# Kernel optimization log

Measured on AMD Instinct MI355X. Metric: run time of the kernel, lower is better.

Reference implementation:

```python
import jax, jax.numpy as jnp
import numpy as np

INPUT_DIM = 4
HIDDEN_DIM = 256
T_OBS, T_UNOBS, BATCH = 64, 32, 4096


def setup_inputs() -> dict:
    key = jax.random.key(0)
    ks = jax.random.split(key, 16)
    H, D = HIDDEN_DIM, INPUT_DIM
    s = lambda k, shape, fan: jax.random.normal(k, shape, jnp.float32) * (1.0 / np.sqrt(fan))
    return {
        "x_obs": jax.random.normal(ks[0], (T_OBS, BATCH, D), jnp.float32),
        "t_obs": jnp.cumsum(jax.random.uniform(ks[1], (T_OBS, BATCH, 1), jnp.float32), axis=0),
        "t_unobs": jax.random.uniform(ks[2], (T_UNOBS, BATCH, 1), jnp.float32),
        # stem MLP (n_layers=2): Linear(D+1 -> H), LeakyReLU, Linear(H -> H)
        "stem_w1": s(ks[3], (H, D + 1), D + 1),
        "stem_b1": jnp.zeros((H,), jnp.float32),
        "stem_w2": s(ks[4], (H, H), H),
        "stem_b2": jnp.zeros((H,), jnp.float32),
        # single-layer GRU, PyTorch gate order (r, z, n)
        "gru_wi": s(ks[5], (3 * H, H), H),
        "gru_wh": s(ks[6], (3 * H, H), H),
        "gru_bi": jnp.zeros((3 * H,), jnp.float32),
        "gru_bh": jnp.zeros((3 * H,), jnp.float32),
        # head MLP (n_layers=1): Linear(H -> D)
        "head_w": s(ks[7], (D, H), H),
        "head_b": jnp.zeros((D,), jnp.float32),
    }


def _gru_cell(x, h, wi, wh, bi, bh):
    # x, h: [B, H].  PyTorch GRU: r,z gates sigmoid; n gate tanh with r gating hidden path.
    gx = x @ wi.T + bi
    gh = h @ wh.T + bh
    rx, zx, nx = jnp.split(gx, 3, axis=-1)
    rh, zh, nh = jnp.split(gh, 3, axis=-1)
    r = jax.nn.sigmoid(rx + rh)
    u = jax.nn.sigmoid(zx + zh)
    n = jnp.tanh(nx + r * nh)
    return (1.0 - u) * n + u * h


def reference(x_obs, t_obs, t_unobs, stem_w1, stem_b1, stem_w2, stem_b2,
              gru_wi, gru_wh, gru_bi, gru_bh, head_w, head_b):
    unobs_len = t_unobs.shape[0]
    batch, hidden = x_obs.shape[1], gru_wh.shape[1]

    # preprocess: first difference of time (0 at step 0), concat, stem MLP
    t_diff = jnp.concatenate([jnp.zeros_like(t_obs[:1]), t_obs[1:] - t_obs[:-1]], axis=0)
    xt = jnp.concatenate([x_obs, t_diff], axis=-1)             # [T_obs, B, D+1]
    xt = jax.nn.leaky_relu(xt @ stem_w1.T + stem_b1)
    xt = xt @ stem_w2.T + stem_b2                              # [T_obs, B, H]

    cell = lambda x, h: _gru_cell(x, jax.lax.stop_gradient(h), gru_wi, gru_wh, gru_bi, gru_bh)

    h0 = jnp.zeros((batch, hidden), x_obs.dtype)

    def obs_step(h, x_t):
        h_new = cell(x_t, h)
        return h_new, None

    h, _ = jax.lax.scan(obs_step, h0, xt)
    z_last = h                                                  # output of 1-layer GRU == hidden

    def ar_step(carry, _):
        z, h = carry
        h_new = cell(z, h)
        return (h_new, h_new), h_new

    (_, _), zs_rest = jax.lax.scan(ar_step, (z_last, h), None, length=unobs_len - 1)
    zs = jnp.concatenate([z_last[None], zs_rest], axis=0)       # [T_unobs, B, H]

    x_hats = zs @ head_w.T + head_b                             # [T_unobs, B, D]
    return x_hats, zs
```

## Files before the change

### kernel.cpp

```cpp
#include <hip/hip_runtime.h>
#include <cstdint>
#include <cstddef>

#define T_OBS_C 64
#define T_UNOBS_C 32
#define BATCH_C 4096
#define HID_C 256

typedef short v8s __attribute__((ext_vector_type(8)));
typedef float v4f __attribute__((ext_vector_type(4)));
typedef unsigned short u16x8 __attribute__((ext_vector_type(8)));

__device__ __forceinline__ float bf2f(unsigned short u) {
  union { unsigned int i; float f; } v; v.i = ((unsigned int)u) << 16; return v.f;
}
__device__ __forceinline__ unsigned short f2bf(float f) {
  union { float f; unsigned int i; } v; v.f = f;
  unsigned int r = (v.i + 0x7FFFu + ((v.i >> 16) & 1u)) >> 16;
  return (unsigned short)r;
}

__global__ void prep_kernel(const float* __restrict__ wi,
                            const float* __restrict__ w2,
                            const float* __restrict__ b2,
                            const float* __restrict__ bi,
                            unsigned short* __restrict__ wi_hi,
                            unsigned short* __restrict__ wi_lo,
                            const float* __restrict__ wh,
                            unsigned short* __restrict__ wh_hi,
                            unsigned short* __restrict__ wh_lo,
                            unsigned short* __restrict__ wc_hi,
                            unsigned short* __restrict__ wc_lo,
                            float* __restrict__ bc_obs) {
  const int n = blockIdx.x;
  const int k = threadIdx.x;
  const int idx = n * 256 + k;

  float wv = wi[idx];
  unsigned short h1 = f2bf(wv);
  wi_hi[idx] = h1; wi_lo[idx] = f2bf(wv - bf2f(h1));

  float hv = wh[idx];
  unsigned short h2 = f2bf(hv);
  wh_hi[idx] = h2; wh_lo[idx] = f2bf(hv - bf2f(h2));

  float acc = 0.f;
  for (int j = 0; j < 256; ++j)
    acc += wi[n * 256 + j] * w2[j * 256 + k];
  unsigned short h3 = f2bf(acc);
  wc_hi[idx] = h3; wc_lo[idx] = f2bf(acc - bf2f(h3));

  if (k == 0) {
    float b = 0.f;
    for (int j = 0; j < 256; ++j) b += wi[n * 256 + j] * b2[j];
    bc_obs[n] = b + bi[n];
  }
}

__global__ __launch_bounds__(512, 2)
void rnn_xcd(const float* __restrict__ x_obs,
             const float* __restrict__ t_obs,
             const float* __restrict__ w1,
             const float* __restrict__ b1,
             const unsigned short* __restrict__ wc_hi, const unsigned short* __restrict__ wc_lo,
             const unsigned short* __restrict__ wi_hi, const unsigned short* __restrict__ wi_lo,
             const unsigned short* __restrict__ wh_hi, const unsigned short* __restrict__ wh_lo,
             const float* __restrict__ bc_obs,
             const float* __restrict__ bi,
             const float* __restrict__ bh,
             const float* __restrict__ head_w,
             const float* __restrict__ head_b,
             unsigned short* h_hi0, unsigned short* h_lo0,
             unsigned short* h_hi1, unsigned short* h_lo1,
             unsigned short* st_hi0, unsigned short* st_lo0,
             unsigned short* st_hi1, unsigned short* st_lo1,
             unsigned int* cnt,
             float* out_x,
             float* out_z) {
  __shared__ unsigned short wlds[73728];

  const int tid = threadIdx.x;
  const int bid = blockIdx.x;
  const int jj  = bid & 15;
  const int cg  = bid >> 4;
  const int rg  = ((jj & 7) << 1) | (jj >> 3);
  const int m0  = rg << 8;
  const int c0  = cg << 4;

  {
    const unsigned short* srcs[6] = {wc_hi, wc_lo, wi_hi, wi_lo, wh_hi, wh_lo};
    for (int id = tid; id < 9216; id += 512) {
      const int sub = id >> 9;
      const int mat = sub / 6;
      const int g   = (sub >> 1) % 3;
      const int hl  = sub & 1;
      const int within = id & 511;
      const int row = within >> 5;
      const int c16 = within & 31;
      const unsigned short* s = srcs[mat * 2 + hl] +
          (((size_t)(g * 256 + c0 + row)) << 8) + (c16 << 3);
      u16x8 v = *(const u16x8*)s;
      *(u16x8*)(wlds + (sub << 12) + (row << 8) + ((c16 ^ row) << 3)) = v;
    }
  }

  const int wave = tid >> 6;
  const int lane = tid & 63;
  const int quad = lane >> 4;
  const int l16  = lane & 15;
  const int jc   = c0 + l16;

  float xb_o[3], xb_a[3], hb_[3], hwv[4];
  #pragma unroll
  for (int g = 0; g < 3; ++g) {
    xb_o[g] = bc_obs[g * 256 + jc];
    xb_a[g] = bi[g * 256 + jc];
    hb_[g]  = bh[g * 256 + jc];
  }
  #pragma unroll
  for (int d = 0; d < 4; ++d) hwv[d] = head_w[d * 256 + jc];

  const size_t rowA0 = (size_t)(m0 + (wave * 2 + 0) * 16 + l16) << 8;
  const size_t rowA1 = (size_t)(m0 + (wave * 2 + 1) * 16 + l16) << 8;

  auto stem_slice = [&](int tt, unsigned short* dh, unsigned short* dl) {
    const int row  = tid >> 1;
    const int half = tid & 1;
    const size_t grow = (size_t)(m0 + row);
    const size_t xo = (size_t)tt * BATCH_C + grow;
    const float4 xv = *(const float4*)(x_obs + xo * 4);
    float td = 0.f;
    if (tt > 0) td = t_obs[xo] - t_obs[xo - BATCH_C];
    const int j0 = c0 + half * 8;
    u16x8 hi8, lo8;
    #pragma unroll
    for (int j = 0; j < 8; ++j) {
      const int jg = j0 + j;
      const float* wr = w1 + jg * 5;
      float pre = xv.x * wr[0] + xv.y * wr[1] + xv.z * wr[2] +
                  xv.w * wr[3] + td * wr[4] + b1[jg];
      float a = (pre > 0.f) ? pre : 0.01f * pre;
      unsigned short h = f2bf(a);
      hi8[j] = h; lo8[j] = f2bf(a - bf2f(h));
    }
    *(u16x8*)(dh + (grow << 8) + j0) = hi8;
    *(u16x8*)(dl + (grow << 8) + j0) = lo8;
  };

  auto rgbar = [&](unsigned int epoch) {
    __syncthreads();
    if (tid == 0) {
      unsigned int* c = cnt + (rg << 6);
      __hip_atomic_fetch_add(c, 1u, __ATOMIC_RELEASE, __HIP_MEMORY_SCOPE_AGENT);
      const unsigned int tgt = epoch << 4;
      while (__hip_atomic_load(c, __ATOMIC_ACQUIRE, __HIP_MEMORY_SCOPE_AGENT) < tgt)
        __builtin_amdgcn_s_sleep(2);
    }
    __syncthreads();
  };

  stem_slice(0, st_hi0, st_lo0);
  rgbar(1);

  unsigned int epoch = 2;
  #pragma unroll 1
  for (int step = 0; step < T_OBS_C + T_UNOBS_C - 1; ++step) {
    const bool obs = (step < T_OBS_C);
    const unsigned short* hih = (step & 1) ? h_hi1 : h_hi0;
    const unsigned short* hil = (step & 1) ? h_lo1 : h_lo0;
    unsigned short* hoh = (step & 1) ? h_hi0 : h_hi1;
    unsigned short* hol = (step & 1) ? h_lo0 : h_lo1;
    const unsigned short* sxh = obs ? ((step & 1) ? st_hi1 : st_hi0) : hih;
    const unsigned short* sxl = obs ? ((step & 1) ? st_lo1 : st_lo0) : hil;
    const int matx = obs ? 0 : 1;
    const int zi = (step == T_OBS_C - 1) ? 0
                   : (step >= T_OBS_C ? step - (T_OBS_C - 1) : -1);

    v4f aX[2][3], aH[2][3];
    #pragma unroll
    for (int mt = 0; mt < 2; ++mt)
      #pragma unroll
      for (int g = 0; g < 3; ++g) {
        aX[mt][g] = (v4f){0.f, 0.f, 0.f, 0.f};
        aH[mt][g] = (v4f){0.f, 0.f, 0.f, 0.f};
      }

    #pragma unroll
    for (int kc = 0; kc < 8; ++kc) {
      const size_t ko = (size_t)(kc * 32 + quad * 8);
      v8s ax0h = *(const v8s*)(sxh + rowA0 + ko);
      v8s ax0l = *(const v8s*)(sxl + rowA0 + ko);
      v8s ax1h = *(const v8s*)(sxh + rowA1 + ko);
      v8s ax1l = *(const v8s*)(sxl + rowA1 + ko);
      v8s ah0h, ah0l, ah1h, ah1l;
      if (obs) {
        ah0h = *(const v8s*)(hih + rowA0 + ko);
        ah0l = *(const v8s*)(hil + rowA0 + ko);
        ah1h = *(const v8s*)(hih + rowA1 + ko);
        ah1l = *(const v8s*)(hil + rowA1 + ko);
      } else {
        ah0h = ax0h; ah0l = ax0l; ah1h = ax1h; ah1l = ax1l;
      }
      const int lrow = (l16 << 8) + ((((kc * 4 + quad) ^ l16)) << 3);
      #pragma unroll
      for (int g = 0; g < 3; ++g) {
        const v8s bxh = *(const v8s*)(wlds + (((matx * 3 + g) * 2 + 0) << 12) + lrow);
        const v8s bxl = *(const v8s*)(wlds + (((matx * 3 + g) * 2 + 1) << 12) + lrow);
        const v8s bhh = *(const v8s*)(wlds + (((6 + g) * 2 + 0) << 12) + lrow);
        const v8s bhl = *(const v8s*)(wlds + (((6 + g) * 2 + 1) << 12) + lrow);
        aX[0][g] = __builtin_amdgcn_mfma_f32_16x16x32_bf16(ax0h, bxh, aX[0][g], 0, 0, 0);
        aX[0][g] = __builtin_amdgcn_mfma_f32_16x16x32_bf16(ax0l, bxh, aX[0][g], 0, 0, 0);
        aX[0][g] = __builtin_amdgcn_mfma_f32_16x16x32_bf16(ax0h, bxl, aX[0][g], 0, 0, 0);
        aX[1][g] = __builtin_amdgcn_mfma_f32_16x16x32_bf16(ax1h, bxh, aX[1][g], 0, 0, 0);
        aX[1][g] = __builtin_amdgcn_mfma_f32_16x16x32_bf16(ax1l, bxh, aX[1][g], 0, 0, 0);
        aX[1][g] = __builtin_amdgcn_mfma_f32_16x16x32_bf16(ax1h, bxl, aX[1][g], 0, 0, 0);
        aH[0][g] = __builtin_amdgcn_mfma_f32_16x16x32_bf16(ah0h, bhh, aH[0][g], 0, 0, 0);
        aH[0][g] = __builtin_amdgcn_mfma_f32_16x16x32_bf16(ah0l, bhh, aH[0][g], 0, 0, 0);
        aH[0][g] = __builtin_amdgcn_mfma_f32_16x16x32_bf16(ah0h, bhl, aH[0][g], 0, 0, 0);
        aH[1][g] = __builtin_amdgcn_mfma_f32_16x16x32_bf16(ah1h, bhh, aH[1][g], 0, 0, 0);
        aH[1][g] = __builtin_amdgcn_mfma_f32_16x16x32_bf16(ah1l, bhh, aH[1][g], 0, 0, 0);
        aH[1][g] = __builtin_amdgcn_mfma_f32_16x16x32_bf16(ah1h, bhl, aH[1][g], 0, 0, 0);
      }
    }

    #pragma unroll
    for (int mt = 0; mt < 2; ++mt) {
      #pragma unroll
      for (int r = 0; r < 4; ++r) {
        const int grow = m0 + (wave * 2 + mt) * 16 + quad * 4 + r;
        const size_t hoff = ((size_t)grow << 8) + jc;
        const float xbr = obs ? xb_o[0] : xb_a[0];
        const float xbz = obs ? xb_o[1] : xb_a[1];
        const float xbn = obs ? xb_o[2] : xb_a[2];
        float gr = aX[mt][0][r] + xbr + aH[mt][0][r] + hb_[0];
        float gz = aX[mt][1][r] + xbz + aH[mt][1][r] + hb_[1];
        float nx = aX[mt][2][r] + xbn;
        float nh = aH[mt][2][r] + hb_[2];
        float rr = 1.f / (1.f + expf(-gr));
        float uu = 1.f / (1.f + expf(-gz));
        float nn = tanhf(nx + rr * nh);
        float hold = bf2f(hih[hoff]) + bf2f(hil[hoff]);
        float hnew = (1.f - uu) * nn + uu * hold;
        unsigned short hi = f2bf(hnew);
        hoh[hoff] = hi;
        hol[hoff] = f2bf(hnew - bf2f(hi));
        if (zi >= 0) {
          out_z[((size_t)zi << 20) + hoff] = hnew;
          #pragma unroll
          for (int d = 0; d < 4; ++d) {
            float pd = hnew * hwv[d];
            pd += __shfl_xor(pd, 1);
            pd += __shfl_xor(pd, 2);
            pd += __shfl_xor(pd, 4);
            pd += __shfl_xor(pd, 8);
            if (l16 == 0) {
              if (cg == 0) pd += head_b[d];
              atomicAdd(out_x + ((((size_t)zi << 12) + grow) << 2) + d, pd);
            }
          }
        }
      }
    }

    if (obs && step + 1 < T_OBS_C)
      stem_slice(step + 1, ((step + 1) & 1) ? st_hi1 : st_hi0,
                           ((step + 1) & 1) ? st_lo1 : st_lo0);

    if (step < T_OBS_C + T_UNOBS_C - 2) rgbar(epoch++);
  }
}

extern "C" void kernel_launch(void* const* d_in, const int* in_sizes, int n_in,
                              void* d_out, int out_size, void* d_ws, size_t ws_size,
                              hipStream_t stream) {
  const float* x_obs = (const float*)d_in[0];
  const float* t_obs = (const float*)d_in[1];
  const float* w1 = (const float*)d_in[3];
  const float* b1 = (const float*)d_in[4];
  const float* w2 = (const float*)d_in[5];
  const float* b2 = (const float*)d_in[6];
  const float* wi = (const float*)d_in[7];
  const float* wh = (const float*)d_in[8];
  const float* bi = (const float*)d_in[9];
  const float* bh = (const float*)d_in[10];
  const float* hw = (const float*)d_in[11];
  const float* hb = (const float*)d_in[12];

  float* out_x = (float*)d_out;
  float* out_z = out_x + (size_t)T_UNOBS_C * BATCH_C * 4;

  unsigned short* p = (unsigned short*)d_ws;
  unsigned short* wi_hi = p; p += 768 * 256;
  unsigned short* wi_lo = p; p += 768 * 256;
  unsigned short* wh_hi = p; p += 768 * 256;
  unsigned short* wh_lo = p; p += 768 * 256;
  unsigned short* wc_hi = p; p += 768 * 256;
  unsigned short* wc_lo = p; p += 768 * 256;
  unsigned short* h_hi0 = p; p += (size_t)1 << 20;
  unsigned short* h_lo0 = p; p += (size_t)1 << 20;
  unsigned short* h_hi1 = p; p += (size_t)1 << 20;
  unsigned short* h_lo1 = p; p += (size_t)1 << 20;
  unsigned short* st_hi0 = p; p += (size_t)1 << 20;
  unsigned short* st_lo0 = p; p += (size_t)1 << 20;
  unsigned short* st_hi1 = p; p += (size_t)1 << 20;
  unsigned short* st_lo1 = p; p += (size_t)1 << 20;
  float* bc_obs = (float*)p; p += 768 * 2;
  unsigned int* cnt = (unsigned int*)p;

  hipMemsetAsync(h_hi0, 0, (size_t)4 << 20, stream);
  hipMemsetAsync(cnt, 0, 16 * 64 * sizeof(unsigned int), stream);
  hipMemsetAsync(out_x, 0, (size_t)T_UNOBS_C * BATCH_C * 4 * sizeof(float), stream);

  prep_kernel<<<768, 256, 0, stream>>>(wi, w2, b2, bi,
                                       wi_hi, wi_lo, wh, wh_hi, wh_lo,
                                       wc_hi, wc_lo, bc_obs);

  void* args[] = {
    (void*)&x_obs, (void*)&t_obs, (void*)&w1, (void*)&b1,
    (void*)&wc_hi, (void*)&wc_lo, (void*)&wi_hi, (void*)&wi_lo,
    (void*)&wh_hi, (void*)&wh_lo,
    (void*)&bc_obs, (void*)&bi, (void*)&bh, (void*)&hw, (void*)&hb,
    (void*)&h_hi0, (void*)&h_lo0, (void*)&h_hi1, (void*)&h_lo1,
    (void*)&st_hi0, (void*)&st_lo0, (void*)&st_hi1, (void*)&st_lo1,
    (void*)&cnt, (void*)&out_x, (void*)&out_z
  };
  hipLaunchCooperativeKernel(reinterpret_cast<void*>(rnn_xcd),
                             dim3(256), dim3(512), args, 0, stream);
}
```

Before: 3.288 ms.

## Compute stem activations in registers and precompute next-step input projection off critical path

Each wave now computes the stem LeakyReLU activations for its own rows directly in registers, using w1 and b1 copied into shared memory, instead of writing bf16 hi/lo stem slices to global buffers and reading them back. The input-path MFMA accumulation for step t+1 is run after step t's gate update and before the grid barrier, so each observed step only does the hidden-path matmul after the barrier. This removes the global round trip for the stem buffers and shortens the post-barrier critical path. In exchange each wave recomputes the stem for its K slice, and holding the extra aXp accumulators raises register pressure.

```diff
diff --git a/kernel.cpp b/kernel.cpp
--- a/kernel.cpp
+++ b/kernel.cpp
@@ -58,7 +58,7 @@
 }
 
 __global__ __launch_bounds__(512, 2)
-void rnn_xcd(const float* __restrict__ x_obs,
+void rnn_ws2(const float* __restrict__ x_obs,
              const float* __restrict__ t_obs,
              const float* __restrict__ w1,
              const float* __restrict__ b1,
@@ -72,12 +72,12 @@
              const float* __restrict__ head_b,
              unsigned short* h_hi0, unsigned short* h_lo0,
              unsigned short* h_hi1, unsigned short* h_lo1,
-             unsigned short* st_hi0, unsigned short* st_lo0,
-             unsigned short* st_hi1, unsigned short* st_lo1,
              unsigned int* cnt,
              float* out_x,
              float* out_z) {
   __shared__ unsigned short wlds[73728];
+  __shared__ float w1t[1280];
+  __shared__ float b1s[256];
 
   const int tid = threadIdx.x;
   const int bid = blockIdx.x;
@@ -102,6 +102,11 @@
       u16x8 v = *(const u16x8*)s;
       *(u16x8*)(wlds + (sub << 12) + (row << 8) + ((c16 ^ row) << 3)) = v;
     }
+    for (int i = tid; i < 1280; i += 512) {
+      const int k = i / 5, j = i - k * 5;
+      w1t[j * 256 + k] = w1[i];
+    }
+    if (tid < 256) b1s[tid] = b1[tid];
   }
 
   const int wave = tid >> 6;
@@ -120,32 +125,10 @@
   #pragma unroll
   for (int d = 0; d < 4; ++d) hwv[d] = head_w[d * 256 + jc];
 
-  const size_t rowA0 = (size_t)(m0 + (wave * 2 + 0) * 16 + l16) << 8;
-  const size_t rowA1 = (size_t)(m0 + (wave * 2 + 1) * 16 + l16) << 8;
-
-  auto stem_slice = [&](int tt, unsigned short* dh, unsigned short* dl) {
-    const int row  = tid >> 1;
-    const int half = tid & 1;
-    const size_t grow = (size_t)(m0 + row);
-    const size_t xo = (size_t)tt * BATCH_C + grow;
-    const float4 xv = *(const float4*)(x_obs + xo * 4);
-    float td = 0.f;
-    if (tt > 0) td = t_obs[xo] - t_obs[xo - BATCH_C];
-    const int j0 = c0 + half * 8;
-    u16x8 hi8, lo8;
-    #pragma unroll
-    for (int j = 0; j < 8; ++j) {
-      const int jg = j0 + j;
-      const float* wr = w1 + jg * 5;
-      float pre = xv.x * wr[0] + xv.y * wr[1] + xv.z * wr[2] +
-                  xv.w * wr[3] + td * wr[4] + b1[jg];
-      float a = (pre > 0.f) ? pre : 0.01f * pre;
-      unsigned short h = f2bf(a);
-      hi8[j] = h; lo8[j] = f2bf(a - bf2f(h));
-    }
-    *(u16x8*)(dh + (grow << 8) + j0) = hi8;
-    *(u16x8*)(dl + (grow << 8) + j0) = lo8;
-  };
+  const int rowL0 = (wave * 2 + 0) * 16 + l16;
+  const int rowL1 = (wave * 2 + 1) * 16 + l16;
+  const size_t rowA0 = (size_t)(m0 + rowL0) << 8;
+  const size_t rowA1 = (size_t)(m0 + rowL1) << 8;
 
   auto rgbar = [&](unsigned int epoch) {
     __syncthreads();
@@ -159,7 +142,62 @@
     __syncthreads();
   };
 
-  stem_slice(0, st_hi0, st_lo0);
+  __syncthreads();
+
+  float4 xv0, xv1; float td0 = 0.f, td1 = 0.f;
+  auto load_x = [&](int tt) {
+    const size_t xo0 = (size_t)tt * BATCH_C + m0 + rowL0;
+    const size_t xo1 = (size_t)tt * BATCH_C + m0 + rowL1;
+    xv0 = *(const float4*)(x_obs + xo0 * 4);
+    xv1 = *(const float4*)(x_obs + xo1 * 4);
+    if (tt > 0) {
+      td0 = t_obs[xo0] - t_obs[xo0 - BATCH_C];
+      td1 = t_obs[xo1] - t_obs[xo1 - BATCH_C];
+    } else { td0 = 0.f; td1 = 0.f; }
+  };
+
+  v4f aXp[2][3];
+  auto xpath_pre = [&]() {
+    #pragma unroll
+    for (int mt = 0; mt < 2; ++mt)
+      #pragma unroll
+      for (int g = 0; g < 3; ++g)
+        aXp[mt][g] = (v4f){0.f, 0.f, 0.f, 0.f};
+    #pragma unroll
+    for (int kc = 0; kc < 8; ++kc) {
+      v8s s0h, s0l, s1h, s1l;
+      #pragma unroll
+      for (int j = 0; j < 8; ++j) {
+        const int k = kc * 32 + quad * 8 + j;
+        const float wA = w1t[k], wB = w1t[256 + k], wC = w1t[512 + k],
+                    wD = w1t[768 + k], wE = w1t[1024 + k];
+        const float bb = b1s[k];
+        float p0 = xv0.x * wA + xv0.y * wB + xv0.z * wC + xv0.w * wD + td0 * wE + bb;
+        float a0 = (p0 > 0.f) ? p0 : 0.01f * p0;
+        unsigned short h0 = f2bf(a0);
+        s0h[j] = h0; s0l[j] = f2bf(a0 - bf2f(h0));
+        float p1 = xv1.x * wA + xv1.y * wB + xv1.z * wC + xv1.w * wD + td1 * wE + bb;
+        float a1 = (p1 > 0.f) ? p1 : 0.01f * p1;
+        unsigned short h1 = f2bf(a1);
+        s1h[j] = h1; s1l[j] = f2bf(a1 - bf2f(h1));
+      }
+      const int lrow = (l16 << 8) + ((((kc * 4 + quad) ^ l16)) << 3);
+      #pragma unroll
+      for (int g = 0; g < 3; ++g) {
+        const v8s bxh = *(const v8s*)(wlds + ((g * 2 + 0) << 12) + lrow);
+        const v8s bxl = *(const v8s*)(wlds + ((g * 2 + 1) << 12) + lrow);
+        aXp[0][g] = __builtin_amdgcn_mfma_f32_16x16x32_bf16(s0h, bxh, aXp[0][g], 0, 0, 0);
+        aXp[0][g] = __builtin_amdgcn_mfma_f32_16x16x32_bf16(s0l, bxh, aXp[0][g], 0, 0, 0);
+        aXp[0][g] = __builtin_amdgcn_mfma_f32_16x16x32_bf16(s0h, bxl, aXp[0][g], 0, 0, 0);
+        aXp[1][g] = __builtin_amdgcn_mfma_f32_16x16x32_bf16(s1h, bxh, aXp[1][g], 0, 0, 0);
+        aXp[1][g] = __builtin_amdgcn_mfma_f32_16x16x32_bf16(s1l, bxh, aXp[1][g], 0, 0, 0);
+        aXp[1][g] = __builtin_amdgcn_mfma_f32_16x16x32_bf16(s1h, bxl, aXp[1][g], 0, 0, 0);
+      }
+    }
+  };
+
+  load_x(0);
+  xpath_pre();
   rgbar(1);
 
   unsigned int epoch = 2;
@@ -170,9 +208,6 @@
     const unsigned short* hil = (step & 1) ? h_lo1 : h_lo0;
     unsigned short* hoh = (step & 1) ? h_hi0 : h_hi1;
     unsigned short* hol = (step & 1) ? h_lo0 : h_lo1;
-    const unsigned short* sxh = obs ? ((step & 1) ? st_hi1 : st_hi0) : hih;
-    const unsigned short* sxl = obs ? ((step & 1) ? st_lo1 : st_lo0) : hil;
-    const int matx = obs ? 0 : 1;
     const int zi = (step == T_OBS_C - 1) ? 0
                    : (step >= T_OBS_C ? step - (T_OBS_C - 1) : -1);
 
@@ -181,45 +216,62 @@
     for (int mt = 0; mt < 2; ++mt)
       #pragma unroll
       for (int g = 0; g < 3; ++g) {
-        aX[mt][g] = (v4f){0.f, 0.f, 0.f, 0.f};
+        aX[mt][g] = obs ? aXp[mt][g] : (v4f){0.f, 0.f, 0.f, 0.f};
         aH[mt][g] = (v4f){0.f, 0.f, 0.f, 0.f};
       }
 
-    #pragma unroll
-    for (int kc = 0; kc < 8; ++kc) {
-      const size_t ko = (size_t)(kc * 32 + quad * 8);
-      v8s ax0h = *(const v8s*)(sxh + rowA0 + ko);
-      v8s ax0l = *(const v8s*)(sxl + rowA0 + ko);
-      v8s ax1h = *(const v8s*)(sxh + rowA1 + ko);
-      v8s ax1l = *(const v8s*)(sxl + rowA1 + ko);
-      v8s ah0h, ah0l, ah1h, ah1l;
-      if (obs) {
-        ah0h = *(const v8s*)(hih + rowA0 + ko);
-        ah0l = *(const v8s*)(hil + rowA0 + ko);
-        ah1h = *(const v8s*)(hih + rowA1 + ko);
-        ah1l = *(const v8s*)(hil + rowA1 + ko);
-      } else {
-        ah0h = ax0h; ah0l = ax0l; ah1h = ax1h; ah1l = ax1l;
-      }
-      const int lrow = (l16 << 8) + ((((kc * 4 + quad) ^ l16)) << 3);
-      #pragma unroll
-      for (int g = 0; g < 3; ++g) {
-        const v8s bxh = *(const v8s*)(wlds + (((matx * 3 + g) * 2 + 0) << 12) + lrow);
-        const v8s bxl = *(const v8s*)(wlds + (((matx * 3 + g) * 2 + 1) << 12) + lrow);
-        const v8s bhh = *(const v8s*)(wlds + (((6 + g) * 2 + 0) << 12) + lrow);
-        const v8s bhl = *(const v8s*)(wlds + (((6 + g) * 2 + 1) << 12) + lrow);
-        aX[0][g] = __builtin_amdgcn_mfma_f32_16x16x32_bf16(ax0h, bxh, aX[0][g], 0, 0, 0);
-        aX[0][g] = __builtin_amdgcn_mfma_f32_16x16x32_bf16(ax0l, bxh, aX[0][g], 0, 0, 0);
-        aX[0][g] = __builtin_amdgcn_mfma_f32_16x16x32_bf16(ax0h, bxl, aX[0][g], 0, 0, 0);
-        aX[1][g] = __builtin_amdgcn_mfma_f32_16x16x32_bf16(ax1h, bxh, aX[1][g], 0, 0, 0);
-        aX[1][g] = __builtin_amdgcn_mfma_f32_16x16x32_bf16(ax1l, bxh, aX[1][g], 0, 0, 0);
-        aX[1][g] = __builtin_amdgcn_mfma_f32_16x16x32_bf16(ax1h, bxl, aX[1][g], 0, 0, 0);
-        aH[0][g] = __builtin_amdgcn_mfma_f32_16x16x32_bf16(ah0h, bhh, aH[0][g], 0, 0, 0);
-        aH[0][g] = __builtin_amdgcn_mfma_f32_16x16x32_bf16(ah0l, bhh, aH[0][g], 0, 0, 0);
-        aH[0][g] = __builtin_amdgcn_mfma_f32_16x16x32_bf16(ah0h, bhl, aH[0][g], 0, 0, 0);
-        aH[1][g] = __builtin_amdgcn_mfma_f32_16x16x32_bf16(ah1h, bhh, aH[1][g], 0, 0, 0);
-        aH[1][g] = __builtin_amdgcn_mfma_f32_16x16x32_bf16(ah1l, bhh, aH[1][g], 0, 0, 0);
-        aH[1][g] = __builtin_amdgcn_mfma_f32_16x16x32_bf16(ah1h, bhl, aH[1][g], 0, 0, 0);
+    const bool nextobs = (step + 1 < T_OBS_C);
+    if (nextobs) load_x(step + 1);
+
+    if (obs) {
+      #pragma unroll
+      for (int kc = 0; kc < 8; ++kc) {
+        const size_t ko = (size_t)(kc * 32 + quad * 8);
+        const v8s ah0h = *(const v8s*)(hih + rowA0 + ko);
+        const v8s ah0l = *(const v8s*)(hil + rowA0 + ko);
+        const v8s ah1h = *(const v8s*)(hih + rowA1 + ko);
+        const v8s ah1l = *(const v8s*)(hil + rowA1 + ko);
+        const int lrow = (l16 << 8) + ((((kc * 4 + quad) ^ l16)) << 3);
+        #pragma unroll
+        for (int g = 0; g < 3; ++g) {
+          const v8s bhh = *(const v8s*)(wlds + (((6 + g) * 2 + 0) << 12) + lrow);
+          const v8s bhl = *(const v8s*)(wlds + (((6 + g) * 2 + 1) << 12) + lrow);
+          aH[0][g] = __builtin_amdgcn_mfma_f32_16x16x32_bf16(ah0h, bhh, aH[0][g], 0, 0, 0);
+          aH[0][g] = __builtin_amdgcn_mfma_f32_16x16x32_bf16(ah0l, bhh, aH[0][g], 0, 0, 0);
+          aH[0][g] = __builtin_amdgcn_mfma_f32_16x16x32_bf16(ah0h, bhl, aH[0][g], 0, 0, 0);
+          aH[1][g] = __builtin_amdgcn_mfma_f32_16x16x32_bf16(ah1h, bhh, aH[1][g], 0, 0, 0);
+          aH[1][g] = __builtin_amdgcn_mfma_f32_16x16x32_bf16(ah1l, bhh, aH[1][g], 0, 0, 0);
+          aH[1][g] = __builtin_amdgcn_mfma_f32_16x16x32_bf16(ah1h, bhl, aH[1][g], 0, 0, 0);
+        }
+      }
+    } else {
+      #pragma unroll
+      for (int kc = 0; kc < 8; ++kc) {
+        const size_t ko = (size_t)(kc * 32 + quad * 8);
+        const v8s ah0h = *(const v8s*)(hih + rowA0 + ko);
+        const v8s ah0l = *(const v8s*)(hil + rowA0 + ko);
+        const v8s ah1h = *(const v8s*)(hih + rowA1 + ko);
+        const v8s ah1l = *(const v8s*)(hil + rowA1 + ko);
+        const int lrow = (l16 << 8) + ((((kc * 4 + quad) ^ l16)) << 3);
+        #pragma unroll
+        for (int g = 0; g < 3; ++g) {
+          const v8s bxh = *(const v8s*)(wlds + (((3 + g) * 2 + 0) << 12) + lrow);
+          const v8s bxl = *(const v8s*)(wlds + (((3 + g) * 2 + 1) << 12) + lrow);
+          const v8s bhh = *(const v8s*)(wlds + (((6 + g) * 2 + 0) << 12) + lrow);
+          const v8s bhl = *(const v8s*)(wlds + (((6 + g) * 2 + 1) << 12) + lrow);
+          aX[0][g] = __builtin_amdgcn_mfma_f32_16x16x32_bf16(ah0h, bxh, aX[0][g], 0, 0, 0);
+          aX[0][g] = __builtin_amdgcn_mfma_f32_16x16x32_bf16(ah0l, bxh, aX[0][g], 0, 0, 0);
+          aX[0][g] = __builtin_amdgcn_mfma_f32_16x16x32_bf16(ah0h, bxl, aX[0][g], 0, 0, 0);
+          aX[1][g] = __builtin_amdgcn_mfma_f32_16x16x32_bf16(ah1h, bxh, aX[1][g], 0, 0, 0);
+          aX[1][g] = __builtin_amdgcn_mfma_f32_16x16x32_bf16(ah1l, bxh, aX[1][g], 0, 0, 0);
+          aX[1][g] = __builtin_amdgcn_mfma_f32_16x16x32_bf16(ah1h, bxl, aX[1][g], 0, 0, 0);
+          aH[0][g] = __builtin_amdgcn_mfma_f32_16x16x32_bf16(ah0h, bhh, aH[0][g], 0, 0, 0);
+          aH[0][g] = __builtin_amdgcn_mfma_f32_16x16x32_bf16(ah0l, bhh, aH[0][g], 0, 0, 0);
+          aH[0][g] = __builtin_amdgcn_mfma_f32_16x16x32_bf16(ah0h, bhl, aH[0][g], 0, 0, 0);
+          aH[1][g] = __builtin_amdgcn_mfma_f32_16x16x32_bf16(ah1h, bhh, aH[1][g], 0, 0, 0);
+          aH[1][g] = __builtin_amdgcn_mfma_f32_16x16x32_bf16(ah1l, bhh, aH[1][g], 0, 0, 0);
+          aH[1][g] = __builtin_amdgcn_mfma_f32_16x16x32_bf16(ah1h, bhl, aH[1][g], 0, 0, 0);
+        }
       }
     }
 
@@ -262,9 +314,7 @@
       }
     }
 
-    if (obs && step + 1 < T_OBS_C)
-      stem_slice(step + 1, ((step + 1) & 1) ? st_hi1 : st_hi0,
-                           ((step + 1) & 1) ? st_lo1 : st_lo0);
+    if (nextobs) xpath_pre();
 
     if (step < T_OBS_C + T_UNOBS_C - 2) rgbar(epoch++);
   }
@@ -300,10 +350,6 @@
   unsigned short* h_lo0 = p; p += (size_t)1 << 20;
   unsigned short* h_hi1 = p; p += (size_t)1 << 20;
   unsigned short* h_lo1 = p; p += (size_t)1 << 20;
-  unsigned short* st_hi0 = p; p += (size_t)1 << 20;
-  unsigned short* st_lo0 = p; p += (size_t)1 << 20;
-  unsigned short* st_hi1 = p; p += (size_t)1 << 20;
-  unsigned short* st_lo1 = p; p += (size_t)1 << 20;
   float* bc_obs = (float*)p; p += 768 * 2;
   unsigned int* cnt = (unsigned int*)p;
 
@@ -321,9 +367,8 @@
     (void*)&wh_hi, (void*)&wh_lo,
     (void*)&bc_obs, (void*)&bi, (void*)&bh, (void*)&hw, (void*)&hb,
     (void*)&h_hi0, (void*)&h_lo0, (void*)&h_hi1, (void*)&h_lo1,
-    (void*)&st_hi0, (void*)&st_lo0, (void*)&st_hi1, (void*)&st_lo1,
     (void*)&cnt, (void*)&out_x, (void*)&out_z
   };
-  hipLaunchCooperativeKernel(reinterpret_cast<void*>(rnn_xcd),
+  hipLaunchCooperativeKernel(reinterpret_cast<void*>(rnn_ws2),
                              dim3(256), dim3(512), args, 0, stream);
 }
```

After: 2.873 ms. -12.6%, faster.
